# Performance work log

Hardware: AMD Instinct MI355X
Metric: run time of the kernel (lower is better)

## Reference

```python
import jax, jax.numpy as jnp
import numpy as np

GROUPS = 32
EPS = 1e-3  # keras GroupNormalization default epsilon


def setup_inputs() -> dict:
    key = jax.random.key(0)
    ks = jax.random.split(key, 7)
    B, H, W, C = 16, 32, 32, 512
    inputs = jax.random.normal(ks[0], (B, H, W, C), dtype=jnp.float32)
    gamma = jnp.ones((C,), dtype=jnp.float32)
    beta = jnp.zeros((C,), dtype=jnp.float32)
    # EinsumDense 'bhwc,cae->bhwae', output last dims (C,3), bias axes 'ae'
    W_qkv = jax.random.normal(ks[1], (C, C, 3), dtype=jnp.float32) / np.sqrt(C)
    b_qkv = jnp.zeros((C, 3), dtype=jnp.float32)
    # EinsumDense 'bhwc,cd->bhwd', bias axes 'd'
    W_out = jax.random.normal(ks[2], (C, C), dtype=jnp.float32) / np.sqrt(C)
    b_out = jnp.zeros((C,), dtype=jnp.float32)
    return {
        "inputs": inputs,
        "gamma": gamma,
        "beta": beta,
        "W_qkv": W_qkv,
        "b_qkv": b_qkv,
        "W_out": W_out,
        "b_out": b_out,
    }


def group_norm(x, gamma, beta):
    B, H, W, C = x.shape
    g = GROUPS
    xr = x.reshape(B, H, W, g, C // g)
    mean = jnp.mean(xr, axis=(1, 2, 4), keepdims=True)
    var = jnp.var(xr, axis=(1, 2, 4), keepdims=True)
    xn = (xr - mean) * jax.lax.rsqrt(var + EPS)
    return xn.reshape(B, H, W, C) * gamma + beta


def reference(inputs, gamma, beta, W_qkv, b_qkv, W_out, b_out):
    B, H, W, C = inputs.shape
    scale = C ** (-0.5)
    x = group_norm(inputs, gamma, beta)
    # QKV projection: bhwc,cae->bhwae  (+ bias over 'ae')
    qkv = jnp.einsum("bhwc,cae->bhwae", x, W_qkv) + b_qkv
    q, k, v = qkv[..., 0], qkv[..., 1], qkv[..., 2]  # each [B,H,W,C]
    # full spatial attention: [B,H,W,H,W]
    attn = jnp.einsum("bhwc,btlc->bhwtl", q, k) * scale
    attn = attn.reshape(B, H, W, H * W)
    attn = jax.nn.softmax(attn, axis=-1)
    attn = attn.reshape(B, H, W, H, W)
    out = jnp.einsum("bhwtl,btlc->bhwc", attn, v)
    out = jnp.einsum("bhwc,cd->bhwd", out, W_out) + b_out
    return inputs + out
```

## Files before the change

kernel.cpp:

```cpp
#include <hip/hip_runtime.h>
#include <hip/hip_bf16.h>

#define NB    16
#define SP    1024
#define NC    512
#define NG    32
#define MTOT  (NB*SP)
#define EPSV  1e-3f
#define SCALE 0.04419417382415922f

using f32x4   = __attribute__((ext_vector_type(4))) float;
using short8  = __attribute__((ext_vector_type(8))) short;
using short4v = __attribute__((ext_vector_type(4))) short;
using bf16x8v = __attribute__((ext_vector_type(8))) __bf16;

__device__ __forceinline__ unsigned short f2bf(float f) {
  union { float f; unsigned int u; } x; x.f = f;
  unsigned int u = x.u;
  unsigned int r = (u + 0x7FFFu + ((u >> 16) & 1u)) >> 16;
  return (unsigned short)r;
}
__device__ __forceinline__ float bf2f(unsigned short b) {
  union { unsigned int u; float f; } x; x.u = ((unsigned int)b) << 16;
  return x.f;
}

#define GLOAD_LDS16(g, l)                                                     \
  __builtin_amdgcn_global_load_lds(                                           \
      (const __attribute__((address_space(1))) void*)(g),                     \
      (__attribute__((address_space(3))) void*)(l), 16, 0, 0)

__global__ __launch_bounds__(256) void gn_stats_k(const float* __restrict__ x,
                                                  float2* __restrict__ stats) {
  int bg = blockIdx.x;
  int b = bg >> 5, g = bg & 31;
  int tid = threadIdx.x;
  int c = tid & 15, s0 = tid >> 4;
  const float* base = x + (long)b * SP * NC + g * 16 + c;
  float s = 0.f, ss = 0.f;
  for (int sp = s0; sp < SP; sp += 16) {
    float v = base[(long)sp * NC];
    s += v; ss += v * v;
  }
  for (int o = 32; o > 0; o >>= 1) { s += __shfl_xor(s, o); ss += __shfl_xor(ss, o); }
  __shared__ float rs[4], rss[4];
  int lane = tid & 63, wv = tid >> 6;
  if (lane == 0) { rs[wv] = s; rss[wv] = ss; }
  __syncthreads();
  if (tid == 0) {
    float S = rs[0] + rs[1] + rs[2] + rs[3];
    float SS = rss[0] + rss[1] + rss[2] + rss[3];
    float mean = S * (1.f / 16384.f);
    float var  = SS * (1.f / 16384.f) - mean * mean;
    stats[bg] = make_float2(mean, rsqrtf(var + EPSV));
  }
}

__global__ __launch_bounds__(256) void gn_apply_k(const float* __restrict__ x,
                                                  const float2* __restrict__ stats,
                                                  const float* __restrict__ gamma,
                                                  const float* __restrict__ beta,
                                                  unsigned short* __restrict__ xn) {
  long t = (long)blockIdx.x * 256 + threadIdx.x;
  long base = t * 8;
  int c = (int)(base & 511);
  int b = (int)(base >> 19);
  float2 st = stats[b * NG + (c >> 4)];
  f32x4 v0 = *reinterpret_cast<const f32x4*>(x + base);
  f32x4 v1 = *reinterpret_cast<const f32x4*>(x + base + 4);
  f32x4 g0 = *reinterpret_cast<const f32x4*>(gamma + c);
  f32x4 g1 = *reinterpret_cast<const f32x4*>(gamma + c + 4);
  f32x4 b0 = *reinterpret_cast<const f32x4*>(beta + c);
  f32x4 b1 = *reinterpret_cast<const f32x4*>(beta + c + 4);
  short8 o;
  #pragma unroll
  for (int q = 0; q < 4; ++q) {
    float sc = st.y * g0[q];
    o[q] = (short)f2bf(v0[q] * sc + (b0[q] - st.x * sc));
  }
  #pragma unroll
  for (int q = 0; q < 4; ++q) {
    float sc = st.y * g1[q];
    o[q + 4] = (short)f2bf(v1[q] * sc + (b1[q] - st.x * sc));
  }
  *reinterpret_cast<short8*>(xn + base) = o;
}

__global__ __launch_bounds__(256) void pack_wqkv_k(const float* __restrict__ W,
                                                   const float* __restrict__ bq,
                                                   unsigned short* __restrict__ Wp,
                                                   float* __restrict__ bp) {
  int idx = blockIdx.x * 256 + threadIdx.x;
  int n = idx >> 9, c = idx & 511;
  int e = n >> 9, a = n & 511;
  Wp[idx] = f2bf(W[((long)c * 512 + a) * 3 + e]);
  if (idx < 1536) {
    int e2 = idx >> 9, a2 = idx & 511;
    bp[idx] = bq[a2 * 3 + e2];
  }
}

__global__ __launch_bounds__(256) void pack_wout_k(const float* __restrict__ W,
                                                   unsigned short* __restrict__ Wp) {
  int idx = blockIdx.x * 256 + threadIdx.x;
  int n = idx >> 9, c = idx & 511;
  Wp[idx] = f2bf(W[(long)c * 512 + n]);
}

__global__ void transpose_v_k(const unsigned short* __restrict__ qkv,
                              unsigned short* __restrict__ vT) {
  __shared__ unsigned short t[32][33];
  int bs = blockIdx.x, bc = blockIdx.y, b = blockIdx.z;
  int tx = threadIdx.x, ty = threadIdx.y;
  #pragma unroll
  for (int k = 0; k < 4; ++k) {
    int s = bs * 32 + ty + k * 8, c = bc * 32 + tx;
    t[ty + k * 8][tx] = qkv[((long)b * SP + s) * 1536 + 1024 + c];
  }
  __syncthreads();
  #pragma unroll
  for (int k = 0; k < 4; ++k) {
    int c = bc * 32 + ty + k * 8, s = bs * 32 + tx;
    vT[((long)b * NC + c) * SP + s] = t[tx][ty + k * 8];
  }
}

__global__ __launch_bounds__(256) void softmax_k(unsigned short* __restrict__ S) {
  long row = blockIdx.x;
  unsigned short* r = S + row * 1024;
  int tid = threadIdx.x, lane = tid & 63, wv = tid >> 6;
  short4v raw = *reinterpret_cast<const short4v*>(r + tid * 4);
  float v[4];
  #pragma unroll
  for (int q = 0; q < 4; ++q) v[q] = bf2f((unsigned short)raw[q]);
  float m = fmaxf(fmaxf(v[0], v[1]), fmaxf(v[2], v[3]));
  for (int o = 32; o > 0; o >>= 1) m = fmaxf(m, __shfl_xor(m, o));
  __shared__ float wm[4], ws[4];
  if (lane == 0) wm[wv] = m;
  __syncthreads();
  float rmax = fmaxf(fmaxf(wm[0], wm[1]), fmaxf(wm[2], wm[3]));
  float e[4]; float ssum = 0.f;
  #pragma unroll
  for (int q = 0; q < 4; ++q) { e[q] = __expf(v[q] - rmax); ssum += e[q]; }
  for (int o = 32; o > 0; o >>= 1) ssum += __shfl_xor(ssum, o);
  if (lane == 0) ws[wv] = ssum;
  __syncthreads();
  float inv = 1.f / (ws[0] + ws[1] + ws[2] + ws[3]);
  short4v pv;
  #pragma unroll
  for (int q = 0; q < 4; ++q) pv[q] = (short)f2bf(e[q] * inv);
  *reinterpret_cast<short4v*>(r + tid * 4) = pv;
}

template <int EPI>
__global__ __launch_bounds__(512, 2) void gemm8(
    const unsigned short* __restrict__ Ap, long strideA, int lda,
    const unsigned short* __restrict__ Bp, long strideB, int ldb,
    void* __restrict__ Op, long strideO, int ldo,
    const float* __restrict__ bias, const float* __restrict__ residual,
    int K, float scale) {
  constexpr int SLOT = 24576;
  extern __shared__ unsigned char smem[];
  const int tid = threadIdx.x;
  const int lane = tid & 63, wv = tid >> 6;
  const int wm2 = wv >> 2, wn4 = wv & 3;

  const int nwg  = gridDim.x * gridDim.y;
  const int flat = blockIdx.y * gridDim.x + blockIdx.x;
  const int w    = (flat & 7) * (nwg >> 3) + (flat >> 3);
  const int bn = (w % gridDim.x) * 256;
  const int bm = (w / gridDim.x) * 128;
  const int z = blockIdx.z;
  const unsigned short* Ag = Ap + (long)z * strideA;
  const unsigned short* Bg = Bp + (long)z * strideB;

  long offA;
  { int sid = tid, sr = sid >> 3, sl = (sid & 7) ^ (sr & 7);
    offA = (long)(bm + sr * 2 + (sl >> 2)) * lda + (sl & 3) * 8; }
  long offB0, offB1;
  { int sid = tid, sr = sid >> 3, sl = (sid & 7) ^ (sr & 7);
    offB0 = (long)(bn + sr * 2 + (sl >> 2)) * ldb + (sl & 3) * 8;
    sid = 512 + tid; sr = sid >> 3; sl = (sid & 7) ^ (sr & 7);
    offB1 = (long)(bn + sr * 2 + (sl >> 2)) * ldb + (sl & 3) * 8; }
  const int ldsA_off  = wv * 1024;
  const int ldsB0_off = 8192 + wv * 1024;
  const int ldsB1_off = 16384 + wv * 1024;

  int aoff[4], boff[4];
  #pragma unroll
  for (int i = 0; i < 4; ++i) {
    int r = wm2 * 64 + i * 16 + (lane & 15);
    int sr = r >> 1, sl = ((r & 1) * 4 + (lane >> 4)) ^ (sr & 7);
    aoff[i] = sr * 128 + sl * 16;
  }
  #pragma unroll
  for (int j = 0; j < 4; ++j) {
    int r = wn4 * 64 + j * 16 + (lane & 15);
    int sr = r >> 1, sl = ((r & 1) * 4 + (lane >> 4)) ^ (sr & 7);
    boff[j] = 8192 + sr * 128 + sl * 16;
  }

  const int NT = K >> 5;
  #pragma unroll
  for (int t = 0; t < 3; ++t) {
    int sb = t * SLOT, kt = t * 32;
    GLOAD_LDS16(Ag + offA + kt,  smem + sb + ldsA_off);
    GLOAD_LDS16(Bg + offB0 + kt, smem + sb + ldsB0_off);
    GLOAD_LDS16(Bg + offB1 + kt, smem + sb + ldsB1_off);
  }
  asm volatile("s_waitcnt vmcnt(6)" ::: "memory");
  __builtin_amdgcn_s_barrier();

  f32x4 acc[4][4] = {};
  for (int t = 0; t < NT; ++t) {
    const unsigned char* sa = smem + (t & 3) * SLOT;
    short8 av[4], bv[4];
    #pragma unroll
    for (int i = 0; i < 4; ++i)
      av[i] = *reinterpret_cast<const short8*>(sa + aoff[i]);
    #pragma unroll
    for (int j = 0; j < 4; ++j)
      bv[j] = *reinterpret_cast<const short8*>(sa + boff[j]);
    if (t + 3 < NT) {
      int sb = ((t + 3) & 3) * SLOT, kt = (t + 3) * 32;
      GLOAD_LDS16(Ag + offA + kt,  smem + sb + ldsA_off);
      GLOAD_LDS16(Bg + offB0 + kt, smem + sb + ldsB0_off);
      GLOAD_LDS16(Bg + offB1 + kt, smem + sb + ldsB1_off);
    }
    __builtin_amdgcn_s_barrier();
    asm volatile("s_waitcnt lgkmcnt(0)" ::: "memory");
    __builtin_amdgcn_sched_barrier(0);
    __builtin_amdgcn_s_setprio(1);
    #pragma unroll
    for (int i = 0; i < 4; ++i)
      #pragma unroll
      for (int j = 0; j < 4; ++j)
        acc[i][j] = __builtin_amdgcn_mfma_f32_16x16x32_bf16(
            __builtin_bit_cast(bf16x8v, av[i]),
            __builtin_bit_cast(bf16x8v, bv[j]), acc[i][j], 0, 0, 0);
    __builtin_amdgcn_s_setprio(0);
    __builtin_amdgcn_sched_barrier(0);
    if (t + 3 < NT) {
      asm volatile("s_waitcnt vmcnt(6)" ::: "memory");
    } else if (t + 2 < NT) {
      asm volatile("s_waitcnt vmcnt(3)" ::: "memory");
    } else {
      asm volatile("s_waitcnt vmcnt(0)" ::: "memory");
    }
    __builtin_amdgcn_s_barrier();
  }

  const int colb = bn + wn4 * 64 + (lane & 15);
  const int rowb = bm + wm2 * 64 + (lane >> 4) * 4;
  #pragma unroll
  for (int i = 0; i < 4; ++i) {
    #pragma unroll
    for (int r = 0; r < 4; ++r) {
      int rowg = rowb + i * 16 + r;
      #pragma unroll
      for (int j = 0; j < 4; ++j) {
        int colg = colb + j * 16;
        float v = acc[i][j][r];
        if (EPI == 0) {
          v += bias[colg];
          ((unsigned short*)Op)[(long)z * strideO + (long)rowg * ldo + colg] = f2bf(v);
        } else if (EPI == 2) {
          ((unsigned short*)Op)[(long)z * strideO + (long)rowg * ldo + colg] = f2bf(v * scale);
        } else {
          v += bias[colg] + residual[(long)rowg * ldo + colg];
          ((float*)Op)[(long)rowg * ldo + colg] = v;
        }
      }
    }
  }
}

extern "C" void kernel_launch(void* const* d_in, const int* in_sizes, int n_in,
                              void* d_out, int out_size, void* d_ws, size_t ws_size,
                              hipStream_t stream) {
  const float* x     = (const float*)d_in[0];
  const float* gamma = (const float*)d_in[1];
  const float* beta  = (const float*)d_in[2];
  const float* Wqkv  = (const float*)d_in[3];
  const float* bqkv  = (const float*)d_in[4];
  const float* Wout  = (const float*)d_in[5];
  const float* bout  = (const float*)d_in[6];
  float* out = (float*)d_out;

  char* ws = (char*)d_ws;
  float2*         stats = (float2*)(ws + 0);
  unsigned short* wqkvP = (unsigned short*)(ws + 4096);
  float*          bqP   = (float*)(ws + 1576960);
  unsigned short* woutT = (unsigned short*)(ws + 1583104);
  unsigned short* qkv   = (unsigned short*)(ws + 2107392);
  unsigned short* vT    = (unsigned short*)(ws + 52439040);
  unsigned short* Sbuf  = (unsigned short*)(ws + 69216256);
  unsigned short* attn  = (unsigned short*)(ws + 136325120);
  unsigned short* xn    = (unsigned short*)(ws + 153102336);

  (void)hipFuncSetAttribute((const void*)gemm8<0>,
        hipFuncAttributeMaxDynamicSharedMemorySize, 98304);
  (void)hipFuncSetAttribute((const void*)gemm8<2>,
        hipFuncAttributeMaxDynamicSharedMemorySize, 98304);
  (void)hipFuncSetAttribute((const void*)gemm8<3>,
        hipFuncAttributeMaxDynamicSharedMemorySize, 98304);

  gn_stats_k<<<512, 256, 0, stream>>>(x, stats);
  gn_apply_k<<<4096, 256, 0, stream>>>(x, stats, gamma, beta, xn);
  pack_wqkv_k<<<3072, 256, 0, stream>>>(Wqkv, bqkv, wqkvP, bqP);
  pack_wout_k<<<1024, 256, 0, stream>>>(Wout, woutT);

  gemm8<0><<<dim3(6, 128, 1), 512, 98304, stream>>>(
      xn, 0L, NC, wqkvP, 0L, NC, qkv, 0L, 1536,
      bqP, nullptr, NC, 1.f);

  transpose_v_k<<<dim3(32, 16, 16), dim3(32, 8), 0, stream>>>(qkv, vT);

  gemm8<2><<<dim3(4, 8, 16), 512, 98304, stream>>>(
      qkv, (long)SP * 1536, 1536, qkv + 512, (long)SP * 1536, 1536,
      Sbuf, (long)SP * SP, SP, nullptr, nullptr, NC, SCALE);

  softmax_k<<<MTOT, 256, 0, stream>>>(Sbuf);

  gemm8<2><<<dim3(2, 8, 16), 512, 98304, stream>>>(
      Sbuf, (long)SP * SP, SP, vT, (long)NC * SP, SP,
      attn, (long)SP * NC, NC, nullptr, nullptr, SP, 1.f);

  gemm8<3><<<dim3(2, 128, 1), 512, 98304, stream>>>(
      attn, 0L, NC, woutT, 0L, NC, out, 0L, NC,
      bout, x, NC, 1.f);
}
```

Before: 279.6 us.

## Double-buffer LDS fragment reads in GEMM main loop, overlapping reads with MFMA

Restructures the bf16 GEMM K-loop into a two-step unrolled ping-pong. The LDS reads for the next K tile go into a second register set while the MFMAs for the current tile run. This removes the per-iteration lgkmcnt(0) stall before the MFMAs and one barrier per step. The cost is higher VGPR pressure from two sets of fragment registers, plus a retuned vmcnt schedule that has to stay correct at the end of the loop.

```diff
diff --git a/kernel.cpp b/kernel.cpp
--- a/kernel.cpp
+++ b/kernel.cpp
@@ -200,55 +200,71 @@
     boff[j] = 8192 + sr * 128 + sl * 16;
   }
 
+#define STAGE(tt, sb) do { long kt = (long)(tt) * 32;                 \
+    GLOAD_LDS16(Ag + offA + kt,  smem + (sb) + ldsA_off);             \
+    GLOAD_LDS16(Bg + offB0 + kt, smem + (sb) + ldsB0_off);            \
+    GLOAD_LDS16(Bg + offB1 + kt, smem + (sb) + ldsB1_off); } while (0)
+
+#define READS(av, bv, sa) do {                                        \
+    _Pragma("unroll")                                                 \
+    for (int i = 0; i < 4; ++i)                                       \
+      av[i] = *reinterpret_cast<const short8*>((sa) + aoff[i]);       \
+    _Pragma("unroll")                                                 \
+    for (int j = 0; j < 4; ++j)                                       \
+      bv[j] = *reinterpret_cast<const short8*>((sa) + boff[j]); } while (0)
+
+#define MFMA16(av, bv) do {                                           \
+    _Pragma("unroll")                                                 \
+    for (int i = 0; i < 4; ++i)                                       \
+      _Pragma("unroll")                                               \
+      for (int j = 0; j < 4; ++j)                                     \
+        acc[i][j] = __builtin_amdgcn_mfma_f32_16x16x32_bf16(          \
+            __builtin_bit_cast(bf16x8v, av[i]),                       \
+            __builtin_bit_cast(bf16x8v, bv[j]), acc[i][j], 0, 0, 0);  \
+    } while (0)
+
   const int NT = K >> 5;
   #pragma unroll
-  for (int t = 0; t < 3; ++t) {
-    int sb = t * SLOT, kt = t * 32;
-    GLOAD_LDS16(Ag + offA + kt,  smem + sb + ldsA_off);
-    GLOAD_LDS16(Bg + offB0 + kt, smem + sb + ldsB0_off);
-    GLOAD_LDS16(Bg + offB1 + kt, smem + sb + ldsB1_off);
-  }
-  asm volatile("s_waitcnt vmcnt(6)" ::: "memory");
+  for (int t = 0; t < 3; ++t)
+    if (t < NT) STAGE(t, t * SLOT);
+  asm volatile("s_waitcnt vmcnt(3)" ::: "memory");
   __builtin_amdgcn_s_barrier();
-
+  __builtin_amdgcn_sched_barrier(0);
+
+  short8 a0[4], b0[4], a1[4], b1[4];
+  READS(a0, b0, smem);
   f32x4 acc[4][4] = {};
-  for (int t = 0; t < NT; ++t) {
-    const unsigned char* sa = smem + (t & 3) * SLOT;
-    short8 av[4], bv[4];
-    #pragma unroll
-    for (int i = 0; i < 4; ++i)
-      av[i] = *reinterpret_cast<const short8*>(sa + aoff[i]);
-    #pragma unroll
-    for (int j = 0; j < 4; ++j)
-      bv[j] = *reinterpret_cast<const short8*>(sa + boff[j]);
-    if (t + 3 < NT) {
-      int sb = ((t + 3) & 3) * SLOT, kt = (t + 3) * 32;
-      GLOAD_LDS16(Ag + offA + kt,  smem + sb + ldsA_off);
-      GLOAD_LDS16(Bg + offB0 + kt, smem + sb + ldsB0_off);
-      GLOAD_LDS16(Bg + offB1 + kt, smem + sb + ldsB1_off);
-    }
-    __builtin_amdgcn_s_barrier();
-    asm volatile("s_waitcnt lgkmcnt(0)" ::: "memory");
+
+  for (int t = 0; t < NT; t += 2) {
+    if (t + 3 < NT) STAGE(t + 3, ((t + 3) & 3) * SLOT);
+    if (t + 1 < NT) { const unsigned char* sa = smem + ((t + 1) & 3) * SLOT; READS(a1, b1, sa); }
     __builtin_amdgcn_sched_barrier(0);
     __builtin_amdgcn_s_setprio(1);
-    #pragma unroll
-    for (int i = 0; i < 4; ++i)
-      #pragma unroll
-      for (int j = 0; j < 4; ++j)
-        acc[i][j] = __builtin_amdgcn_mfma_f32_16x16x32_bf16(
-            __builtin_bit_cast(bf16x8v, av[i]),
-            __builtin_bit_cast(bf16x8v, bv[j]), acc[i][j], 0, 0, 0);
+    MFMA16(a0, b0);
     __builtin_amdgcn_s_setprio(0);
     __builtin_amdgcn_sched_barrier(0);
-    if (t + 3 < NT) {
-      asm volatile("s_waitcnt vmcnt(6)" ::: "memory");
-    } else if (t + 2 < NT) {
-      asm volatile("s_waitcnt vmcnt(3)" ::: "memory");
-    } else {
-      asm volatile("s_waitcnt vmcnt(0)" ::: "memory");
+    if (t + 3 < NT) asm volatile("s_waitcnt vmcnt(3)" ::: "memory");
+    else            asm volatile("s_waitcnt vmcnt(0)" ::: "memory");
+    __builtin_amdgcn_s_barrier();
+    __builtin_amdgcn_sched_barrier(0);
+
+    if (t + 1 < NT) {
+      if (t + 4 < NT) STAGE(t + 4, ((t + 4) & 3) * SLOT);
+      if (t + 2 < NT) { const unsigned char* sa = smem + ((t + 2) & 3) * SLOT; READS(a0, b0, sa); }
+      __builtin_amdgcn_sched_barrier(0);
+      __builtin_amdgcn_s_setprio(1);
+      MFMA16(a1, b1);
+      __builtin_amdgcn_s_setprio(0);
+      __builtin_amdgcn_sched_barrier(0);
+      if (t + 4 < NT) asm volatile("s_waitcnt vmcnt(3)" ::: "memory");
+      else            asm volatile("s_waitcnt vmcnt(0)" ::: "memory");
+      __builtin_amdgcn_s_barrier();
+      __builtin_amdgcn_sched_barrier(0);
     }
-    __builtin_amdgcn_s_barrier();
-  }
+  }
+#undef STAGE
+#undef READS
+#undef MFMA16
 
   const int colb = bn + wn4 * 64 + (lane & 15);
   const int rowb = bm + wm2 * 64 + (lane >> 4) * 4;
```

Result: no change. 280.3 us (+0.2%).
